# Kernel optimization log

Measured on AMD Instinct MI355X. Metric: run time of the kernel, lower is better.

The kernel has to match this reference:

```python
import jax, jax.numpy as jnp
import numpy as np

# Dimensions (match init_kwargs / input_specs)
B, C, H, W = 16, 16, 64, 64
N = H * W          # num_nodes
D_E = 64           # node_embed_dim
D_H = 128          # gnn_hidden_dim
D_R = 256          # readout_output_dim


def _param(key, shape, fan_in):
    return jax.random.normal(key, shape, jnp.float32) * (1.0 / np.sqrt(fan_in))


def setup_inputs() -> dict:
    key = jax.random.key(0)
    ks = jax.random.split(key, 16)
    inp = {
        "obs": jax.random.normal(ks[0], (B, C, H, W), jnp.float32),
        # node_embedding MLP (2 layers: C -> D_E -> D_E)
        "e1_w": _param(ks[1], (C, D_E), C),   "e1_b": jnp.zeros((D_E,), jnp.float32),
        "e2_w": _param(ks[2], (D_E, D_E), D_E), "e2_b": jnp.zeros((D_E,), jnp.float32),
        # 3 GNN layers (Linear then adjacency aggregation)
        "g1_w": _param(ks[3], (D_E, D_H), D_E), "g1_b": jnp.zeros((D_H,), jnp.float32),
        "g2_w": _param(ks[4], (D_H, D_H), D_H), "g2_b": jnp.zeros((D_H,), jnp.float32),
        "g3_w": _param(ks[5], (D_H, D_H), D_H), "g3_b": jnp.zeros((D_H,), jnp.float32),
        # readout MLP (2 layers: D_H -> 2*D_H -> D_R)
        "r1_w": _param(ks[6], (D_H, 2 * D_H), D_H),   "r1_b": jnp.zeros((2 * D_H,), jnp.float32),
        "r2_w": _param(ks[7], (2 * D_H, D_R), 2 * D_H), "r2_b": jnp.zeros((D_R,), jnp.float32),
    }
    return inp


def _adj_norm():
    # 4-neighbor grid adjacency on an H x W grid, row-normalized (same for every
    # batch element, so build once as (N, N) instead of (B, N, N)).
    idx = jnp.arange(N)
    up = jnp.eye(N, k=-W, dtype=jnp.float32)                      # i > 0
    down = jnp.eye(N, k=W, dtype=jnp.float32)                     # i < H-1
    left = jnp.eye(N, k=-1, dtype=jnp.float32) * ((idx % W) != 0)[:, None]
    right = jnp.eye(N, k=1, dtype=jnp.float32) * ((idx % W) != (W - 1))[:, None]
    adj = up + down + left + right
    return adj / (adj.sum(axis=1, keepdims=True) + 1e-6)


def reference(obs, e1_w, e1_b, e2_w, e2_b,
              g1_w, g1_b, g2_w, g2_b, g3_w, g3_b,
              r1_w, r1_b, r2_w, r2_b):
    relu = jax.nn.relu
    # grid -> graph: (B, C, H, W) -> (B, N, C)
    x = jnp.transpose(obs, (0, 2, 3, 1)).reshape(B, N, C)
    # node embedding MLP (output activation per ding MLP default)
    h = relu(x @ e1_w + e1_b)
    h = relu(h @ e2_w + e2_b)
    A = _adj_norm()  # (N, N)
    for Wg, bg in ((g1_w, g1_b), (g2_w, g2_b), (g3_w, g3_b)):
        support = h @ Wg + bg                      # (B, N, D_H)
        h = relu(jnp.einsum('nm,bmf->bnf', A, support))
    g = h.mean(axis=1)                              # (B, D_H) graph readout
    g = relu(g @ r1_w + r1_b)
    return relu(g @ r2_w + r2_b)                    # (B, D_R)
```

## Files before the change

### kernel.cpp

```cpp
#include <hip/hip_runtime.h>


typedef __attribute__((ext_vector_type(8))) short bf16x8;
typedef __attribute__((ext_vector_type(4))) float f32x4;
#define MFMA(a, b, c) __builtin_amdgcn_mfma_f32_16x16x32_bf16(a, b, c, 0, 0, 0)

__device__ inline void block_sync_lgkm() {
    asm volatile("" ::: "memory");
    __builtin_amdgcn_s_waitcnt(0xC07F);
    __builtin_amdgcn_s_barrier();
    asm volatile("" ::: "memory");
}

__device__ inline ushort bf16h(float x) {
    unsigned u = __float_as_uint(x);
    return (ushort)((u + 0x7fffu + ((u >> 16) & 1u)) >> 16);
}
__device__ inline void split_bf16(float x, ushort& hi, ushort& lo) {
    hi = bf16h(x);
    lo = bf16h(x - __uint_as_float(((unsigned)hi) << 16));
}
__device__ inline unsigned pack_split(float x) {
    unsigned u = __float_as_uint(x);
    unsigned hi = (u + 0x7fffu + ((u >> 16) & 1u)) >> 16;
    float r = x - __uint_as_float(hi << 16);
    return (hi << 16) | (__float_as_uint(r) >> 16);
}
__device__ inline void frag_packed(const unsigned* bp, bf16x8& bh, bf16x8& bl) {
    unsigned p[8];
#pragma unroll
    for (int j = 0; j < 8; j++) p[j] = bp[j * 65];
    union { bf16x8 v; unsigned d[4]; } H, L;
#pragma unroll
    for (int j = 0; j < 4; j++) {
        const unsigned e = p[2 * j], o = p[2 * j + 1];
        H.d[j] = (o & 0xFFFF0000u) | (e >> 16);
        L.d[j] = (o << 16) | (e & 0xFFFFu);
    }
    bh = H.v; bl = L.v;
}

__global__ __launch_bounds__(64) void wprep_kernel(
    const float* __restrict__ e1w, const float* __restrict__ e2w,
    const float* __restrict__ g1w, const float* __restrict__ g2w,
    const float* __restrict__ g3w, ushort* __restrict__ wf,
    float* __restrict__ gsum)
{
    const int blk = blockIdx.x, l = threadIdx.x;
    if (blk >= 92) {
        gsum[(blk - 92) * 64 + l] = 0.f;
        return;
    }
    const float* src; int K, N, kc, t; ushort* dst;
    if (blk < 4)        { src = e1w; K = 16;  N = 64;  kc = 0; t = blk;      dst = wf; }
    else if (blk < 12)  { src = e2w; K = 64;  N = 64;  int u = blk - 4;  kc = u >> 2; t = u & 3; dst = wf + 4096; }
    else if (blk < 28)  { src = g1w; K = 64;  N = 128; int u = blk - 12; kc = u >> 3; t = u & 7; dst = wf + 12288; }
    else if (blk < 60)  { src = g2w; K = 128; N = 128; int u = blk - 28; kc = u >> 3; t = u & 7; dst = wf + 28672; }
    else                { src = g3w; K = 128; N = 128; int u = blk - 60; kc = u >> 3; t = u & 7; dst = wf + 61440; }
    const int T = (N == 64) ? 4 : 8;
    ushort* uh = dst + ((kc * T + t) * 2 + 0) * 512 + l * 8;
    ushort* ul = dst + ((kc * T + t) * 2 + 1) * 512 + l * 8;
    const int f = t * 16 + (l & 15);
    const int kb = kc * 32 + ((l >> 4) << 3);
#pragma unroll
    for (int j = 0; j < 8; j++) {
        const int k = kb + j;
        const float w = (k < K) ? src[k * N + f] : 0.f;
        ushort hi, lo; split_bf16(w, hi, lo);
        uh[j] = hi; ul[j] = lo;
    }
}

__global__ __launch_bounds__(256, 4) void embed_kernel(
    const float* __restrict__ obs, const ushort* __restrict__ wf,
    const float* __restrict__ e1b, const float* __restrict__ e2b,
    float* __restrict__ h0)
{
    __shared__ unsigned Xs[32 * 65];
    __shared__ unsigned Hs[64 * 65];
    const int tid = threadIdx.x, b = blockIdx.x >> 6, row = blockIdx.x & 63;
    const int lane = tid & 63, w = tid >> 6, quad = lane >> 4, nl = lane & 15;
    const int cp = tid >> 4, nq = tid & 15;

    const float4 x4 = *(const float4*)(obs + ((size_t)(b * 16 + cp) << 12) + row * 64 + nq * 4);
    unsigned* xp = Xs + cp * 65 + nq * 4;
    xp[0] = pack_split(x4.x); xp[1] = pack_split(x4.y);
    xp[2] = pack_split(x4.z); xp[3] = pack_split(x4.w);
    unsigned* zp = Xs + (16 + cp) * 65 + nq * 4;
    zp[0] = 0u; zp[1] = 0u; zp[2] = 0u; zp[3] = 0u;
    __syncthreads();

    {
        const ushort* wp = wf + lane * 8;
        const bf16x8 wh = *(const bf16x8*)(wp + (w * 2) * 512);
        const bf16x8 wl = *(const bf16x8*)(wp + (w * 2 + 1) * 512);
#pragma unroll
        for (int nt = 0; nt < 4; nt++) {
            const unsigned* bp = Xs + (quad * 8) * 65 + nt * 16 + nl;
            bf16x8 bh, bl; frag_packed(bp, bh, bl);
            f32x4 c = {0.f, 0.f, 0.f, 0.f};
            c = MFMA(wh, bh, c); c = MFMA(wh, bl, c); c = MFMA(wl, bh, c);
#pragma unroll
            for (int reg = 0; reg < 4; reg++) {
                const int fm = 16 * w + quad * 4 + reg;
                Hs[fm * 65 + nt * 16 + nl] = pack_split(fmaxf(c[reg] + e1b[fm], 0.f));
            }
        }
    }
    __syncthreads();

    const ushort* e2f = wf + 4096;
    f32x4 a2[4];
#pragma unroll
    for (int nt = 0; nt < 4; nt++) a2[nt] = (f32x4){0.f, 0.f, 0.f, 0.f};
#pragma unroll
    for (int kc = 0; kc < 2; kc++) {
        const ushort* wp = e2f + lane * 8;
        const bf16x8 wh = *(const bf16x8*)(wp + ((kc * 4 + w) * 2) * 512);
        const bf16x8 wl = *(const bf16x8*)(wp + ((kc * 4 + w) * 2 + 1) * 512);
#pragma unroll
        for (int nt = 0; nt < 4; nt++) {
            const unsigned* bp = Hs + (kc * 32 + quad * 8) * 65 + nt * 16 + nl;
            bf16x8 bh, bl; frag_packed(bp, bh, bl);
            a2[nt] = MFMA(wh, bh, a2[nt]);
            a2[nt] = MFMA(wh, bl, a2[nt]);
            a2[nt] = MFMA(wl, bh, a2[nt]);
        }
    }
#pragma unroll
    for (int reg = 0; reg < 4; reg++) {
        const int f = 16 * w + quad * 4 + reg;
        const float bv = e2b[f];
#pragma unroll
        for (int nt = 0; nt < 4; nt++)
            h0[((size_t)(b * 64 + f) << 12) + row * 64 + nt * 16 + nl] =
                fmaxf(a2[nt][reg] + bv, 0.f);
    }
}

template <int K, bool MEAN>
__global__ __launch_bounds__(256, 4) void gnn_kernel(
    const float* __restrict__ hin, const ushort* __restrict__ wf,
    const float* __restrict__ bias, float* __restrict__ hout,
    float* __restrict__ gsum)
{
    constexpr int NQ = K / 32;
    __shared__ unsigned As[2][32 * 65];
    const int tid = threadIdx.x;
    const int bid = ((blockIdx.x & 7) << 7) | (blockIdx.x >> 3);
    const int b = bid >> 6, row = bid & 63;
    const int lane = tid & 63, w = tid >> 6, quad = lane >> 4, nl = lane & 15;
    const int kp = tid >> 4, nq = tid & 15;
    const float* hb = hin + (size_t)b * K * 4096;
    const int rowu = (row > 0) ? row - 1 : row;
    const int rowd = (row < 63) ? row + 1 : row;
    const float su = (row > 0) ? 1.f : 0.f;
    const float sd = (row < 63) ? 1.f : 0.f;
    float inv[4];
#pragma unroll
    for (int i = 0; i < 4; i++) {
        const int n = nq * 4 + i;
        const int deg = (row > 0) + (row < 63) + (n > 0) + (n < 63);
        inv[i] = 1.f / ((float)deg + 1e-6f);
    }

    const ushort* wfl = wf + lane * 8;
    f32x4 acc[4][2];
#pragma unroll
    for (int nt = 0; nt < 4; nt++) {
        acc[nt][0] = (f32x4){0.f, 0.f, 0.f, 0.f};
        acc[nt][1] = (f32x4){0.f, 0.f, 0.f, 0.f};
    }

    float4 S[2][6];
    bf16x8 V[2][2];

    auto sload = [&](int s, int q) {
#pragma unroll
        for (int it = 0; it < 2; it++) {
            const int kg = q * 32 + it * 16 + kp;
            const float* pk = hb + ((size_t)kg << 12) + nq * 4;
            S[s][it * 3 + 0] = *(const float4*)(pk + row * 64);
            S[s][it * 3 + 1] = *(const float4*)(pk + rowu * 64);
            S[s][it * 3 + 2] = *(const float4*)(pk + rowd * 64);
        }
    };
    auto wload = [&](int q) {
#pragma unroll
        for (int ftl = 0; ftl < 2; ftl++) {
            V[ftl][0] = *(const bf16x8*)(wfl + ((q * 8 + 2 * w + ftl) * 2) * 512);
            V[ftl][1] = *(const bf16x8*)(wfl + ((q * 8 + 2 * w + ftl) * 2 + 1) * 512);
        }
    };
    auto stage = [&](int s, unsigned* Ab) {
#pragma unroll
        for (int it = 0; it < 2; it++) {
            const int kl = it * 16 + kp;
            const float4 c4 = S[s][it * 3 + 0];
            const float4 u4 = S[s][it * 3 + 1];
            const float4 d4 = S[s][it * 3 + 2];
            const float pw = __shfl_up(c4.w, 1);
            const float nx = __shfl_down(c4.x, 1);
            const float lx = (nq > 0) ? pw : 0.f;
            const float rw = (nq < 15) ? nx : 0.f;
            unsigned* ap = Ab + kl * 65 + nq * 4;
            ap[0] = pack_split((su * u4.x + sd * d4.x + lx + c4.y) * inv[0]);
            ap[1] = pack_split((su * u4.y + sd * d4.y + c4.x + c4.z) * inv[1]);
            ap[2] = pack_split((su * u4.z + sd * d4.z + c4.y + c4.w) * inv[2]);
            ap[3] = pack_split((su * u4.w + sd * d4.w + c4.z + rw) * inv[3]);
        }
    };
    auto consume = [&](const unsigned* Ab) {
#pragma unroll
        for (int nt = 0; nt < 4; nt++) {
            const unsigned* bp = Ab + (quad * 8) * 65 + nt * 16 + nl;
            bf16x8 bh, bl; frag_packed(bp, bh, bl);
            acc[nt][0] = MFMA(V[0][0], bh, acc[nt][0]);
            acc[nt][0] = MFMA(V[0][0], bl, acc[nt][0]);
            acc[nt][0] = MFMA(V[0][1], bh, acc[nt][0]);
            acc[nt][1] = MFMA(V[1][0], bh, acc[nt][1]);
            acc[nt][1] = MFMA(V[1][0], bl, acc[nt][1]);
            acc[nt][1] = MFMA(V[1][1], bh, acc[nt][1]);
        }
    };

    wload(0);
    sload(0, 0);
    sload(1, 1);
    stage(0, As[0]);
    block_sync_lgkm();

#pragma unroll
    for (int q = 0; q < NQ; q++) {
        if (q + 2 < NQ) sload(q & 1, q + 2);
        consume(As[q & 1]);
        if (q + 1 < NQ) {
            wload(q + 1);
            stage((q + 1) & 1, As[(q + 1) & 1]);
            block_sync_lgkm();
        }
    }

    if (!MEAN) {
#pragma unroll
        for (int ftl = 0; ftl < 2; ftl++) {
            const int fb = 32 * w + 16 * ftl + quad * 4;
            const float b0 = bias[fb], b1 = bias[fb + 1], b2 = bias[fb + 2], b3 = bias[fb + 3];
#pragma unroll
            for (int nt = 0; nt < 4; nt++) {
                const int n = 16 * nt + nl;
                const int deg = (row > 0) + (row < 63) + (n > 0) + (n < 63);
                const float rs = (float)deg / ((float)deg + 1e-6f);
                float* op = hout + ((size_t)(b * 128 + fb) << 12) + row * 64 + n;
                op[0]        = fmaxf(acc[nt][ftl][0] + rs * b0, 0.f);
                op[1u << 12] = fmaxf(acc[nt][ftl][1] + rs * b1, 0.f);
                op[2u << 12] = fmaxf(acc[nt][ftl][2] + rs * b2, 0.f);
                op[3u << 12] = fmaxf(acc[nt][ftl][3] + rs * b3, 0.f);
            }
        }
    } else {
#pragma unroll
        for (int ftl = 0; ftl < 2; ftl++) {
            const int fb = 32 * w + 16 * ftl + quad * 4;
#pragma unroll
            for (int reg = 0; reg < 4; reg++) {
                const float bv = bias[fb + reg];
                float v = 0.f;
#pragma unroll
                for (int nt = 0; nt < 4; nt++) {
                    const int n = 16 * nt + nl;
                    const int deg = (row > 0) + (row < 63) + (n > 0) + (n < 63);
                    const float rs = (float)deg / ((float)deg + 1e-6f);
                    v += fmaxf(acc[nt][ftl][reg] + rs * bv, 0.f);
                }
                v += __shfl_xor(v, 1); v += __shfl_xor(v, 2);
                v += __shfl_xor(v, 4); v += __shfl_xor(v, 8);
                if (nl == 0) atomicAdd(&gsum[b * 128 + fb + reg], v * (1.f / 4096.f));
            }
        }
    }
}

__global__ __launch_bounds__(256) void readout_kernel(
    const float* __restrict__ gsum, const float* __restrict__ r1w,
    const float* __restrict__ r1b, const float* __restrict__ r2w,
    const float* __restrict__ r2b, float* __restrict__ out)
{
    __shared__ float gs[128];
    __shared__ float g2[256];
    const int b = blockIdx.x, tid = threadIdx.x;
    if (tid < 128) gs[tid] = gsum[b * 128 + tid];
    __syncthreads();
    float a = r1b[tid];
#pragma unroll 16
    for (int k = 0; k < 128; k++) a = fmaf(gs[k], r1w[k * 256 + tid], a);
    g2[tid] = fmaxf(a, 0.f);
    __syncthreads();
    float a2 = r2b[tid];
#pragma unroll 16
    for (int k = 0; k < 256; k++) a2 = fmaf(g2[k], r2w[k * 256 + tid], a2);
    out[b * 256 + tid] = fmaxf(a2, 0.f);
}

extern "C" void kernel_launch(void* const* d_in, const int* in_sizes, int n_in,
                              void* d_out, int out_size, void* d_ws, size_t ws_size,
                              hipStream_t stream)
{
    const float* obs = (const float*)d_in[0];
    const float* e1w = (const float*)d_in[1];
    const float* e1b = (const float*)d_in[2];
    const float* e2w = (const float*)d_in[3];
    const float* e2b = (const float*)d_in[4];
    const float* g1w = (const float*)d_in[5];
    const float* g1b = (const float*)d_in[6];
    const float* g2w = (const float*)d_in[7];
    const float* g2b = (const float*)d_in[8];
    const float* g3w = (const float*)d_in[9];
    const float* g3b = (const float*)d_in[10];
    const float* r1w = (const float*)d_in[11];
    const float* r1b = (const float*)d_in[12];
    const float* r2w = (const float*)d_in[13];
    const float* r2b = (const float*)d_in[14];
    float* out = (float*)d_out;
    float* ws = (float*)d_ws;

    float* h0 = ws;
    float* h1 = ws + 4194304;
    float* h2 = ws + 4194304 + 8388608;
    float* gsum = (float*)((char*)d_ws + 80u * 1024u * 1024u);
    ushort* wfb = (ushort*)((char*)d_ws + 80u * 1024u * 1024u + 8192u);

    hipLaunchKernelGGL(wprep_kernel, dim3(124), dim3(64), 0, stream,
                       e1w, e2w, g1w, g2w, g3w, wfb, gsum);
    hipLaunchKernelGGL(embed_kernel, dim3(1024), dim3(256), 0, stream,
                       obs, wfb, e1b, e2b, h0);
    hipLaunchKernelGGL((gnn_kernel<64, false>), dim3(1024), dim3(256), 0, stream,
                       h0, wfb + 12288, g1b, h1, nullptr);
    hipLaunchKernelGGL((gnn_kernel<128, false>), dim3(1024), dim3(256), 0, stream,
                       h1, wfb + 28672, g2b, h2, nullptr);
    hipLaunchKernelGGL((gnn_kernel<128, true>), dim3(1024), dim3(256), 0, stream,
                       h2, wfb + 61440, g3b, nullptr, gsum);
    hipLaunchKernelGGL(readout_kernel, dim3(16), dim3(256), 0, stream,
                       gsum, r1w, r1b, r2w, r2b, out);
}
```

Before: 161.5 us.

## Fuse weight prep into embed kernel and single-buffer GNN prefetch registers

Merges the weight-preparation launch and the embedding launch into one kernel. The first blocks convert the GNN weights and zero gsum, and every embedding block loads e1/e2 weights into LDS and splits them into bf16 hi/lo fragments itself. This removes one kernel launch and its dependency gap, at the cost of redundant per-block weight conversion. Separately, the GNN kernel's prefetch buffer shrinks from two register sets to one by reordering the load after staging, which cuts register pressure but shortens the distance between prefetch and use.

After: 160.4 us. About the same (-0.6%).

```diff
diff --git a/kernel.cpp b/kernel.cpp
--- a/kernel.cpp
+++ b/kernel.cpp
@@ -40,91 +40,118 @@
     bh = H.v; bl = L.v;
 }
 
-__global__ __launch_bounds__(64) void wprep_kernel(
-    const float* __restrict__ e1w, const float* __restrict__ e2w,
+__global__ __launch_bounds__(256, 4) void prep_embed_kernel(
+    const float* __restrict__ obs,
+    const float* __restrict__ e1w, const float* __restrict__ e1b,
+    const float* __restrict__ e2w, const float* __restrict__ e2b,
     const float* __restrict__ g1w, const float* __restrict__ g2w,
     const float* __restrict__ g3w, ushort* __restrict__ wf,
-    float* __restrict__ gsum)
+    float* __restrict__ gsum, float* __restrict__ h0)
 {
-    const int blk = blockIdx.x, l = threadIdx.x;
-    if (blk >= 92) {
-        gsum[(blk - 92) * 64 + l] = 0.f;
+    const int blk = blockIdx.x, tid = threadIdx.x;
+
+    if (blk < 20) {
+        const int u = blk * 4 + (tid >> 6);
+        const int l = tid & 63;
+        const float* src; int K, kc, t; ushort* dst;
+        if (u < 16)      { src = g1w; K = 64;  kc = u >> 3;        t = u & 7; dst = wf + 12288; }
+        else if (u < 48) { src = g2w; K = 128; kc = (u - 16) >> 3; t = (u - 16) & 7; dst = wf + 28672; }
+        else             { src = g3w; K = 128; kc = (u - 48) >> 3; t = (u - 48) & 7; dst = wf + 61440; }
+        ushort* uh = dst + ((kc * 8 + t) * 2 + 0) * 512 + l * 8;
+        ushort* ul = dst + ((kc * 8 + t) * 2 + 1) * 512 + l * 8;
+        const int f = t * 16 + (l & 15);
+        const int kb = kc * 32 + ((l >> 4) << 3);
+#pragma unroll
+        for (int j = 0; j < 8; j++) {
+            const int k = kb + j;
+            const float w = (k < K) ? src[k * 128 + f] : 0.f;
+            ushort hi, lo; split_bf16(w, hi, lo);
+            uh[j] = hi; ul[j] = lo;
+        }
         return;
     }
-    const float* src; int K, N, kc, t; ushort* dst;
-    if (blk < 4)        { src = e1w; K = 16;  N = 64;  kc = 0; t = blk;      dst = wf; }
-    else if (blk < 12)  { src = e2w; K = 64;  N = 64;  int u = blk - 4;  kc = u >> 2; t = u & 3; dst = wf + 4096; }
-    else if (blk < 28)  { src = g1w; K = 64;  N = 128; int u = blk - 12; kc = u >> 3; t = u & 7; dst = wf + 12288; }
-    else if (blk < 60)  { src = g2w; K = 128; N = 128; int u = blk - 28; kc = u >> 3; t = u & 7; dst = wf + 28672; }
-    else                { src = g3w; K = 128; N = 128; int u = blk - 60; kc = u >> 3; t = u & 7; dst = wf + 61440; }
-    const int T = (N == 64) ? 4 : 8;
-    ushort* uh = dst + ((kc * T + t) * 2 + 0) * 512 + l * 8;
-    ushort* ul = dst + ((kc * T + t) * 2 + 1) * 512 + l * 8;
-    const int f = t * 16 + (l & 15);
-    const int kb = kc * 32 + ((l >> 4) << 3);
-#pragma unroll
-    for (int j = 0; j < 8; j++) {
-        const int k = kb + j;
-        const float w = (k < K) ? src[k * N + f] : 0.f;
-        ushort hi, lo; split_bf16(w, hi, lo);
-        uh[j] = hi; ul[j] = lo;
-    }
-}
-
-__global__ __launch_bounds__(256, 4) void embed_kernel(
-    const float* __restrict__ obs, const ushort* __restrict__ wf,
-    const float* __restrict__ e1b, const float* __restrict__ e2b,
-    float* __restrict__ h0)
-{
-    __shared__ unsigned Xs[32 * 65];
-    __shared__ unsigned Hs[64 * 65];
-    const int tid = threadIdx.x, b = blockIdx.x >> 6, row = blockIdx.x & 63;
+    if (blk < 28) {
+        gsum[(blk - 20) * 256 + tid] = 0.f;
+        return;
+    }
+
+    __shared__ unsigned lds[6240];
+    const int eb = blk - 28, b = eb >> 6, row = eb & 63;
     const int lane = tid & 63, w = tid >> 6, quad = lane >> 4, nl = lane & 15;
     const int cp = tid >> 4, nq = tid & 15;
 
     const float4 x4 = *(const float4*)(obs + ((size_t)(b * 16 + cp) << 12) + row * 64 + nq * 4);
-    unsigned* xp = Xs + cp * 65 + nq * 4;
-    xp[0] = pack_split(x4.x); xp[1] = pack_split(x4.y);
-    xp[2] = pack_split(x4.z); xp[3] = pack_split(x4.w);
-    unsigned* zp = Xs + (16 + cp) * 65 + nq * 4;
-    zp[0] = 0u; zp[1] = 0u; zp[2] = 0u; zp[3] = 0u;
-    __syncthreads();
 
     {
-        const ushort* wp = wf + lane * 8;
-        const bf16x8 wh = *(const bf16x8*)(wp + (w * 2) * 512);
-        const bf16x8 wl = *(const bf16x8*)(wp + (w * 2 + 1) * 512);
-#pragma unroll
-        for (int nt = 0; nt < 4; nt++) {
-            const unsigned* bp = Xs + (quad * 8) * 65 + nt * 16 + nl;
-            bf16x8 bh, bl; frag_packed(bp, bh, bl);
-            f32x4 c = {0.f, 0.f, 0.f, 0.f};
-            c = MFMA(wh, bh, c); c = MFMA(wh, bl, c); c = MFMA(wl, bh, c);
-#pragma unroll
-            for (int reg = 0; reg < 4; reg++) {
-                const int fm = 16 * w + quad * 4 + reg;
-                Hs[fm * 65 + nt * 16 + nl] = pack_split(fmaxf(c[reg] + e1b[fm], 0.f));
+        float* wr = (float*)lds;
+#pragma unroll
+        for (int i = 0; i < 20; i++) {
+            const int idx = tid + 256 * i;
+            wr[idx] = (idx < 1024) ? e1w[idx] : e2w[idx - 1024];
+        }
+    }
+    __syncthreads();
+
+    bf16x8 e1h, e1l, e2h[2], e2l[2];
+    {
+        const float* wr = (const float*)lds;
+        const int f = 16 * w + nl;
+#pragma unroll
+        for (int j = 0; j < 8; j++) {
+            const int k = quad * 8 + j;
+            const float v = (k < 16) ? wr[k * 64 + f] : 0.f;
+            ushort hi, lo; split_bf16(v, hi, lo);
+            e1h[j] = (short)hi; e1l[j] = (short)lo;
+        }
+#pragma unroll
+        for (int kc = 0; kc < 2; kc++)
+#pragma unroll
+            for (int j = 0; j < 8; j++) {
+                const int k = kc * 32 + quad * 8 + j;
+                const float v = wr[1024 + k * 64 + f];
+                ushort hi, lo; split_bf16(v, hi, lo);
+                e2h[kc][j] = (short)hi; e2l[kc][j] = (short)lo;
             }
-        }
-    }
-    __syncthreads();
-
-    const ushort* e2f = wf + 4096;
+    }
+    __syncthreads();
+
+    unsigned* Xs = lds;
+    unsigned* Hs = lds + 2080;
+    {
+        unsigned* xp = Xs + cp * 65 + nq * 4;
+        xp[0] = pack_split(x4.x); xp[1] = pack_split(x4.y);
+        xp[2] = pack_split(x4.z); xp[3] = pack_split(x4.w);
+        unsigned* zp = Xs + (16 + cp) * 65 + nq * 4;
+        zp[0] = 0u; zp[1] = 0u; zp[2] = 0u; zp[3] = 0u;
+    }
+    __syncthreads();
+
+#pragma unroll
+    for (int nt = 0; nt < 4; nt++) {
+        const unsigned* bp = Xs + (quad * 8) * 65 + nt * 16 + nl;
+        bf16x8 bh, bl; frag_packed(bp, bh, bl);
+        f32x4 c = {0.f, 0.f, 0.f, 0.f};
+        c = MFMA(e1h, bh, c); c = MFMA(e1h, bl, c); c = MFMA(e1l, bh, c);
+#pragma unroll
+        for (int reg = 0; reg < 4; reg++) {
+            const int fm = 16 * w + quad * 4 + reg;
+            Hs[fm * 65 + nt * 16 + nl] = pack_split(fmaxf(c[reg] + e1b[fm], 0.f));
+        }
+    }
+    __syncthreads();
+
     f32x4 a2[4];
 #pragma unroll
     for (int nt = 0; nt < 4; nt++) a2[nt] = (f32x4){0.f, 0.f, 0.f, 0.f};
 #pragma unroll
     for (int kc = 0; kc < 2; kc++) {
-        const ushort* wp = e2f + lane * 8;
-        const bf16x8 wh = *(const bf16x8*)(wp + ((kc * 4 + w) * 2) * 512);
-        const bf16x8 wl = *(const bf16x8*)(wp + ((kc * 4 + w) * 2 + 1) * 512);
 #pragma unroll
         for (int nt = 0; nt < 4; nt++) {
             const unsigned* bp = Hs + (kc * 32 + quad * 8) * 65 + nt * 16 + nl;
             bf16x8 bh, bl; frag_packed(bp, bh, bl);
-            a2[nt] = MFMA(wh, bh, a2[nt]);
-            a2[nt] = MFMA(wh, bl, a2[nt]);
-            a2[nt] = MFMA(wl, bh, a2[nt]);
+            a2[nt] = MFMA(e2h[kc], bh, a2[nt]);
+            a2[nt] = MFMA(e2h[kc], bl, a2[nt]);
+            a2[nt] = MFMA(e2l[kc], bh, a2[nt]);
         }
     }
 #pragma unroll
@@ -172,17 +199,17 @@
         acc[nt][1] = (f32x4){0.f, 0.f, 0.f, 0.f};
     }
 
-    float4 S[2][6];
+    float4 S[6];
     bf16x8 V[2][2];
 
-    auto sload = [&](int s, int q) {
+    auto sload = [&](int q) {
 #pragma unroll
         for (int it = 0; it < 2; it++) {
             const int kg = q * 32 + it * 16 + kp;
             const float* pk = hb + ((size_t)kg << 12) + nq * 4;
-            S[s][it * 3 + 0] = *(const float4*)(pk + row * 64);
-            S[s][it * 3 + 1] = *(const float4*)(pk + rowu * 64);
-            S[s][it * 3 + 2] = *(const float4*)(pk + rowd * 64);
+            S[it * 3 + 0] = *(const float4*)(pk + row * 64);
+            S[it * 3 + 1] = *(const float4*)(pk + rowu * 64);
+            S[it * 3 + 2] = *(const float4*)(pk + rowd * 64);
         }
     };
     auto wload = [&](int q) {
@@ -192,13 +219,13 @@
             V[ftl][1] = *(const bf16x8*)(wfl + ((q * 8 + 2 * w + ftl) * 2 + 1) * 512);
         }
     };
-    auto stage = [&](int s, unsigned* Ab) {
+    auto stage = [&](unsigned* Ab) {
 #pragma unroll
         for (int it = 0; it < 2; it++) {
             const int kl = it * 16 + kp;
-            const float4 c4 = S[s][it * 3 + 0];
-            const float4 u4 = S[s][it * 3 + 1];
-            const float4 d4 = S[s][it * 3 + 2];
+            const float4 c4 = S[it * 3 + 0];
+            const float4 u4 = S[it * 3 + 1];
+            const float4 d4 = S[it * 3 + 2];
             const float pw = __shfl_up(c4.w, 1);
             const float nx = __shfl_down(c4.x, 1);
             const float lx = (nq > 0) ? pw : 0.f;
@@ -225,18 +252,18 @@
     };
 
     wload(0);
-    sload(0, 0);
-    sload(1, 1);
-    stage(0, As[0]);
+    sload(0);
+    stage(As[0]);
+    sload(1);
     block_sync_lgkm();
 
 #pragma unroll
     for (int q = 0; q < NQ; q++) {
-        if (q + 2 < NQ) sload(q & 1, q + 2);
         consume(As[q & 1]);
         if (q + 1 < NQ) {
             wload(q + 1);
-            stage((q + 1) & 1, As[(q + 1) & 1]);
+            stage(As[(q + 1) & 1]);
+            if (q + 2 < NQ) sload(q + 2);
             block_sync_lgkm();
         }
     }
@@ -330,10 +357,8 @@
     float* gsum = (float*)((char*)d_ws + 80u * 1024u * 1024u);
     ushort* wfb = (ushort*)((char*)d_ws + 80u * 1024u * 1024u + 8192u);
 
-    hipLaunchKernelGGL(wprep_kernel, dim3(124), dim3(64), 0, stream,
-                       e1w, e2w, g1w, g2w, g3w, wfb, gsum);
-    hipLaunchKernelGGL(embed_kernel, dim3(1024), dim3(256), 0, stream,
-                       obs, wfb, e1b, e2b, h0);
+    hipLaunchKernelGGL(prep_embed_kernel, dim3(1052), dim3(256), 0, stream,
+                       obs, e1w, e1b, e2w, e2b, g1w, g2w, g3w, wfb, gsum, h0);
     hipLaunchKernelGGL((gnn_kernel<64, false>), dim3(1024), dim3(256), 0, stream,
                        h0, wfb + 12288, g1b, h1, nullptr);
     hipLaunchKernelGGL((gnn_kernel<128, false>), dim3(1024), dim3(256), 0, stream,
```

## Split each grid row into two 32-column tiles to double block count

Applied to the files above, without the earlier changes.

Each block in the embed and GNN kernels now handles half a grid row (32 nodes) rather than a full row, so the grid grows from 1024 to 2048 blocks. Shared tiles shrink to 33-column padding and each block holds half as many accumulators. The GNN staging now loads one k-row per thread plus a halo element across the tile boundary, with a shallower prefetch. Launch bounds are raised to 6 blocks per CU, aiming at more occupancy and better latency hiding. The cost is extra halo and up/down-row loads per node, along with a less aggressive software pipeline.

Result: slower. 201.5 us (+24.8%).

```diff
diff --git a/kernel.cpp b/kernel.cpp
--- a/kernel.cpp
+++ b/kernel.cpp
@@ -26,10 +26,11 @@
     float r = x - __uint_as_float(hi << 16);
     return (hi << 16) | (__float_as_uint(r) >> 16);
 }
+template <int ST>
 __device__ inline void frag_packed(const unsigned* bp, bf16x8& bh, bf16x8& bl) {
     unsigned p[8];
 #pragma unroll
-    for (int j = 0; j < 8; j++) p[j] = bp[j * 65];
+    for (int j = 0; j < 8; j++) p[j] = bp[j * ST];
     union { bf16x8 v; unsigned d[4]; } H, L;
 #pragma unroll
     for (int j = 0; j < 4; j++) {
@@ -71,23 +72,27 @@
     }
 }
 
-__global__ __launch_bounds__(256, 4) void embed_kernel(
+__global__ __launch_bounds__(256, 6) void embed_kernel(
     const float* __restrict__ obs, const ushort* __restrict__ wf,
     const float* __restrict__ e1b, const float* __restrict__ e2b,
     float* __restrict__ h0)
 {
-    __shared__ unsigned Xs[32 * 65];
-    __shared__ unsigned Hs[64 * 65];
-    const int tid = threadIdx.x, b = blockIdx.x >> 6, row = blockIdx.x & 63;
+    __shared__ unsigned Xs[32 * 33];
+    __shared__ unsigned Hs[64 * 33];
+    const int blk = blockIdx.x, tid = threadIdx.x;
+    const int bid = ((blk & 7) << 8) | (blk >> 3);
+    const int b = bid >> 7, row = (bid >> 1) & 63, tile = bid & 1;
+    const int gc = tile << 5;
     const int lane = tid & 63, w = tid >> 6, quad = lane >> 4, nl = lane & 15;
     const int cp = tid >> 4, nq = tid & 15;
 
-    const float4 x4 = *(const float4*)(obs + ((size_t)(b * 16 + cp) << 12) + row * 64 + nq * 4);
-    unsigned* xp = Xs + cp * 65 + nq * 4;
-    xp[0] = pack_split(x4.x); xp[1] = pack_split(x4.y);
-    xp[2] = pack_split(x4.z); xp[3] = pack_split(x4.w);
-    unsigned* zp = Xs + (16 + cp) * 65 + nq * 4;
-    zp[0] = 0u; zp[1] = 0u; zp[2] = 0u; zp[3] = 0u;
+    {
+        const float2 x2 = *(const float2*)(obs + ((size_t)(b * 16 + cp) << 12) + row * 64 + gc + nq * 2);
+        Xs[cp * 33 + nq * 2]            = pack_split(x2.x);
+        Xs[cp * 33 + nq * 2 + 1]        = pack_split(x2.y);
+        Xs[(16 + cp) * 33 + nq * 2]     = 0u;
+        Xs[(16 + cp) * 33 + nq * 2 + 1] = 0u;
+    }
     __syncthreads();
 
     {
@@ -95,33 +100,33 @@
         const bf16x8 wh = *(const bf16x8*)(wp + (w * 2) * 512);
         const bf16x8 wl = *(const bf16x8*)(wp + (w * 2 + 1) * 512);
 #pragma unroll
-        for (int nt = 0; nt < 4; nt++) {
-            const unsigned* bp = Xs + (quad * 8) * 65 + nt * 16 + nl;
-            bf16x8 bh, bl; frag_packed(bp, bh, bl);
+        for (int nt = 0; nt < 2; nt++) {
+            const unsigned* bp = Xs + (quad * 8) * 33 + nt * 16 + nl;
+            bf16x8 bh, bl; frag_packed<33>(bp, bh, bl);
             f32x4 c = {0.f, 0.f, 0.f, 0.f};
             c = MFMA(wh, bh, c); c = MFMA(wh, bl, c); c = MFMA(wl, bh, c);
 #pragma unroll
             for (int reg = 0; reg < 4; reg++) {
                 const int fm = 16 * w + quad * 4 + reg;
-                Hs[fm * 65 + nt * 16 + nl] = pack_split(fmaxf(c[reg] + e1b[fm], 0.f));
+                Hs[fm * 33 + nt * 16 + nl] = pack_split(fmaxf(c[reg] + e1b[fm], 0.f));
             }
         }
     }
     __syncthreads();
 
     const ushort* e2f = wf + 4096;
-    f32x4 a2[4];
-#pragma unroll
-    for (int nt = 0; nt < 4; nt++) a2[nt] = (f32x4){0.f, 0.f, 0.f, 0.f};
+    f32x4 a2[2];
+    a2[0] = (f32x4){0.f, 0.f, 0.f, 0.f};
+    a2[1] = (f32x4){0.f, 0.f, 0.f, 0.f};
 #pragma unroll
     for (int kc = 0; kc < 2; kc++) {
         const ushort* wp = e2f + lane * 8;
         const bf16x8 wh = *(const bf16x8*)(wp + ((kc * 4 + w) * 2) * 512);
         const bf16x8 wl = *(const bf16x8*)(wp + ((kc * 4 + w) * 2 + 1) * 512);
 #pragma unroll
-        for (int nt = 0; nt < 4; nt++) {
-            const unsigned* bp = Hs + (kc * 32 + quad * 8) * 65 + nt * 16 + nl;
-            bf16x8 bh, bl; frag_packed(bp, bh, bl);
+        for (int nt = 0; nt < 2; nt++) {
+            const unsigned* bp = Hs + (kc * 32 + quad * 8) * 33 + nt * 16 + nl;
+            bf16x8 bh, bl; frag_packed<33>(bp, bh, bl);
             a2[nt] = MFMA(wh, bh, a2[nt]);
             a2[nt] = MFMA(wh, bl, a2[nt]);
             a2[nt] = MFMA(wl, bh, a2[nt]);
@@ -132,25 +137,27 @@
         const int f = 16 * w + quad * 4 + reg;
         const float bv = e2b[f];
 #pragma unroll
-        for (int nt = 0; nt < 4; nt++)
-            h0[((size_t)(b * 64 + f) << 12) + row * 64 + nt * 16 + nl] =
+        for (int nt = 0; nt < 2; nt++)
+            h0[((size_t)(b * 64 + f) << 12) + row * 64 + gc + nt * 16 + nl] =
                 fmaxf(a2[nt][reg] + bv, 0.f);
     }
 }
 
 template <int K, bool MEAN>
-__global__ __launch_bounds__(256, 4) void gnn_kernel(
+__global__ __launch_bounds__(256, 6) void gnn_kernel(
     const float* __restrict__ hin, const ushort* __restrict__ wf,
     const float* __restrict__ bias, float* __restrict__ hout,
     float* __restrict__ gsum)
 {
     constexpr int NQ = K / 32;
-    __shared__ unsigned As[2][32 * 65];
-    const int tid = threadIdx.x;
-    const int bid = ((blockIdx.x & 7) << 7) | (blockIdx.x >> 3);
-    const int b = bid >> 6, row = bid & 63;
+    __shared__ unsigned As[2][32 * 33];
+    const int blk = blockIdx.x, tid = threadIdx.x;
+    const int bid = ((blk & 7) << 8) | (blk >> 3);
+    const int b = bid >> 7, row = (bid >> 1) & 63, tile = bid & 1;
+    const int gc = tile << 5;
     const int lane = tid & 63, w = tid >> 6, quad = lane >> 4, nl = lane & 15;
-    const int kp = tid >> 4, nq = tid & 15;
+    const int kq = tid >> 3, nq8 = tid & 7, n0 = nq8 * 4;
+    const int hoff = tile ? -1 : 32;
     const float* hb = hin + (size_t)b * K * 4096;
     const int rowu = (row > 0) ? row - 1 : row;
     const int rowd = (row < 63) ? row + 1 : row;
@@ -159,31 +166,29 @@
     float inv[4];
 #pragma unroll
     for (int i = 0; i < 4; i++) {
-        const int n = nq * 4 + i;
+        const int n = gc + n0 + i;
         const int deg = (row > 0) + (row < 63) + (n > 0) + (n < 63);
         inv[i] = 1.f / ((float)deg + 1e-6f);
     }
 
     const ushort* wfl = wf + lane * 8;
-    f32x4 acc[4][2];
-#pragma unroll
-    for (int nt = 0; nt < 4; nt++) {
+    f32x4 acc[2][2];
+#pragma unroll
+    for (int nt = 0; nt < 2; nt++) {
         acc[nt][0] = (f32x4){0.f, 0.f, 0.f, 0.f};
         acc[nt][1] = (f32x4){0.f, 0.f, 0.f, 0.f};
     }
 
-    float4 S[2][6];
+    float4 S0, S1, S2; float S3;
     bf16x8 V[2][2];
 
-    auto sload = [&](int s, int q) {
-#pragma unroll
-        for (int it = 0; it < 2; it++) {
-            const int kg = q * 32 + it * 16 + kp;
-            const float* pk = hb + ((size_t)kg << 12) + nq * 4;
-            S[s][it * 3 + 0] = *(const float4*)(pk + row * 64);
-            S[s][it * 3 + 1] = *(const float4*)(pk + rowu * 64);
-            S[s][it * 3 + 2] = *(const float4*)(pk + rowd * 64);
-        }
+    auto sload = [&](int q) {
+        const int k = q * 32 + kq;
+        const float* pc = hb + ((size_t)k << 12) + row * 64 + gc;
+        S0 = *(const float4*)(pc + n0);
+        S1 = *(const float4*)(hb + ((size_t)k << 12) + rowu * 64 + gc + n0);
+        S2 = *(const float4*)(hb + ((size_t)k << 12) + rowd * 64 + gc + n0);
+        S3 = pc[hoff];
     };
     auto wload = [&](int q) {
 #pragma unroll
@@ -192,29 +197,24 @@
             V[ftl][1] = *(const bf16x8*)(wfl + ((q * 8 + 2 * w + ftl) * 2 + 1) * 512);
         }
     };
-    auto stage = [&](int s, unsigned* Ab) {
-#pragma unroll
-        for (int it = 0; it < 2; it++) {
-            const int kl = it * 16 + kp;
-            const float4 c4 = S[s][it * 3 + 0];
-            const float4 u4 = S[s][it * 3 + 1];
-            const float4 d4 = S[s][it * 3 + 2];
-            const float pw = __shfl_up(c4.w, 1);
-            const float nx = __shfl_down(c4.x, 1);
-            const float lx = (nq > 0) ? pw : 0.f;
-            const float rw = (nq < 15) ? nx : 0.f;
-            unsigned* ap = Ab + kl * 65 + nq * 4;
-            ap[0] = pack_split((su * u4.x + sd * d4.x + lx + c4.y) * inv[0]);
-            ap[1] = pack_split((su * u4.y + sd * d4.y + c4.x + c4.z) * inv[1]);
-            ap[2] = pack_split((su * u4.z + sd * d4.z + c4.y + c4.w) * inv[2]);
-            ap[3] = pack_split((su * u4.w + sd * d4.w + c4.z + rw) * inv[3]);
-        }
+    auto stage = [&](unsigned* Ab) {
+        const float pw = __shfl_up(S0.w, 1);
+        const float nx = __shfl_down(S0.x, 1);
+        const float eL = tile ? S3 : 0.f;
+        const float eR = tile ? 0.f : S3;
+        const float lx = (nq8 > 0) ? pw : eL;
+        const float rw = (nq8 < 7) ? nx : eR;
+        unsigned* ap = Ab + kq * 33 + n0;
+        ap[0] = pack_split((su * S1.x + sd * S2.x + lx + S0.y) * inv[0]);
+        ap[1] = pack_split((su * S1.y + sd * S2.y + S0.x + S0.z) * inv[1]);
+        ap[2] = pack_split((su * S1.z + sd * S2.z + S0.y + S0.w) * inv[2]);
+        ap[3] = pack_split((su * S1.w + sd * S2.w + S0.z + rw) * inv[3]);
     };
     auto consume = [&](const unsigned* Ab) {
 #pragma unroll
-        for (int nt = 0; nt < 4; nt++) {
-            const unsigned* bp = Ab + (quad * 8) * 65 + nt * 16 + nl;
-            bf16x8 bh, bl; frag_packed(bp, bh, bl);
+        for (int nt = 0; nt < 2; nt++) {
+            const unsigned* bp = Ab + (quad * 8) * 33 + nt * 16 + nl;
+            bf16x8 bh, bl; frag_packed<33>(bp, bh, bl);
             acc[nt][0] = MFMA(V[0][0], bh, acc[nt][0]);
             acc[nt][0] = MFMA(V[0][0], bl, acc[nt][0]);
             acc[nt][0] = MFMA(V[0][1], bh, acc[nt][0]);
@@ -225,18 +225,18 @@
     };
 
     wload(0);
-    sload(0, 0);
-    sload(1, 1);
-    stage(0, As[0]);
+    sload(0);
+    stage(As[0]);
+    sload(1);
     block_sync_lgkm();
 
 #pragma unroll
     for (int q = 0; q < NQ; q++) {
-        if (q + 2 < NQ) sload(q & 1, q + 2);
         consume(As[q & 1]);
         if (q + 1 < NQ) {
             wload(q + 1);
-            stage((q + 1) & 1, As[(q + 1) & 1]);
+            stage(As[(q + 1) & 1]);
+            if (q + 2 < NQ) sload(q + 2);
             block_sync_lgkm();
         }
     }
@@ -247,8 +247,8 @@
             const int fb = 32 * w + 16 * ftl + quad * 4;
             const float b0 = bias[fb], b1 = bias[fb + 1], b2 = bias[fb + 2], b3 = bias[fb + 3];
 #pragma unroll
-            for (int nt = 0; nt < 4; nt++) {
-                const int n = 16 * nt + nl;
+            for (int nt = 0; nt < 2; nt++) {
+                const int n = gc + nt * 16 + nl;
                 const int deg = (row > 0) + (row < 63) + (n > 0) + (n < 63);
                 const float rs = (float)deg / ((float)deg + 1e-6f);
                 float* op = hout + ((size_t)(b * 128 + fb) << 12) + row * 64 + n;
@@ -267,8 +267,8 @@
                 const float bv = bias[fb + reg];
                 float v = 0.f;
 #pragma unroll
-                for (int nt = 0; nt < 4; nt++) {
-                    const int n = 16 * nt + nl;
+                for (int nt = 0; nt < 2; nt++) {
+                    const int n = gc + nt * 16 + nl;
                     const int deg = (row > 0) + (row < 63) + (n > 0) + (n < 63);
                     const float rs = (float)deg / ((float)deg + 1e-6f);
                     v += fmaxf(acc[nt][ftl][reg] + rs * bv, 0.f);
@@ -332,13 +332,13 @@
 
     hipLaunchKernelGGL(wprep_kernel, dim3(124), dim3(64), 0, stream,
                        e1w, e2w, g1w, g2w, g3w, wfb, gsum);
-    hipLaunchKernelGGL(embed_kernel, dim3(1024), dim3(256), 0, stream,
+    hipLaunchKernelGGL(embed_kernel, dim3(2048), dim3(256), 0, stream,
                        obs, wfb, e1b, e2b, h0);
-    hipLaunchKernelGGL((gnn_kernel<64, false>), dim3(1024), dim3(256), 0, stream,
+    hipLaunchKernelGGL((gnn_kernel<64, false>), dim3(2048), dim3(256), 0, stream,
                        h0, wfb + 12288, g1b, h1, nullptr);
-    hipLaunchKernelGGL((gnn_kernel<128, false>), dim3(1024), dim3(256), 0, stream,
+    hipLaunchKernelGGL((gnn_kernel<128, false>), dim3(2048), dim3(256), 0, stream,
                        h1, wfb + 28672, g2b, h2, nullptr);
-    hipLaunchKernelGGL((gnn_kernel<128, true>), dim3(1024), dim3(256), 0, stream,
+    hipLaunchKernelGGL((gnn_kernel<128, true>), dim3(2048), dim3(256), 0, stream,
                        h2, wfb + 61440, g3b, nullptr, gsum);
     hipLaunchKernelGGL(readout_kernel, dim3(16), dim3(256), 0, stream,
                        gsum, r1w, r1b, r2w, r2b, out);
```

## Split GNN output features across two blocks and single-buffer the register staging

Applied to the files above, without the earlier changes.

Each GNN block now computes half of the 128 output features, so the grid doubles from 1024 to 2048 blocks, and each wave holds half the accumulators and weight fragments. The register double-buffering of loaded input rows is replaced by a single buffer, reloaded after staging, and launch bounds rise to 6 blocks per CU. The goal is more occupancy and lower register pressure to hide memory latency. The cost is that each block recomputes the same adjacency-aggregated input tile, so input reads and staging work are doubled.

Result: slower. 229.6 us (+42.2%).

```diff
diff --git a/kernel.cpp b/kernel.cpp
--- a/kernel.cpp
+++ b/kernel.cpp
@@ -139,18 +139,20 @@
 }
 
 template <int K, bool MEAN>
-__global__ __launch_bounds__(256, 4) void gnn_kernel(
+__global__ __launch_bounds__(256, 6) void gnn_kernel(
     const float* __restrict__ hin, const ushort* __restrict__ wf,
     const float* __restrict__ bias, float* __restrict__ hout,
     float* __restrict__ gsum)
 {
     constexpr int NQ = K / 32;
     __shared__ unsigned As[2][32 * 65];
-    const int tid = threadIdx.x;
-    const int bid = ((blockIdx.x & 7) << 7) | (blockIdx.x >> 3);
+    const int blk = blockIdx.x, tid = threadIdx.x;
+    const int fh = (blk >> 3) & 1;
+    const int bid = ((blk & 7) << 7) | (blk >> 4);
     const int b = bid >> 6, row = bid & 63;
     const int lane = tid & 63, w = tid >> 6, quad = lane >> 4, nl = lane & 15;
     const int kp = tid >> 4, nq = tid & 15;
+    const int t = fh * 4 + w;
     const float* hb = hin + (size_t)b * K * 4096;
     const int rowu = (row > 0) ? row - 1 : row;
     const int rowd = (row < 63) ? row + 1 : row;
@@ -165,40 +167,34 @@
     }
 
     const ushort* wfl = wf + lane * 8;
-    f32x4 acc[4][2];
-#pragma unroll
-    for (int nt = 0; nt < 4; nt++) {
-        acc[nt][0] = (f32x4){0.f, 0.f, 0.f, 0.f};
-        acc[nt][1] = (f32x4){0.f, 0.f, 0.f, 0.f};
-    }
-
-    float4 S[2][6];
-    bf16x8 V[2][2];
-
-    auto sload = [&](int s, int q) {
+    f32x4 acc[4];
+#pragma unroll
+    for (int nt = 0; nt < 4; nt++) acc[nt] = (f32x4){0.f, 0.f, 0.f, 0.f};
+
+    float4 S[6];
+    bf16x8 V[2];
+
+    auto sload = [&](int q) {
 #pragma unroll
         for (int it = 0; it < 2; it++) {
             const int kg = q * 32 + it * 16 + kp;
             const float* pk = hb + ((size_t)kg << 12) + nq * 4;
-            S[s][it * 3 + 0] = *(const float4*)(pk + row * 64);
-            S[s][it * 3 + 1] = *(const float4*)(pk + rowu * 64);
-            S[s][it * 3 + 2] = *(const float4*)(pk + rowd * 64);
+            S[it * 3 + 0] = *(const float4*)(pk + row * 64);
+            S[it * 3 + 1] = *(const float4*)(pk + rowu * 64);
+            S[it * 3 + 2] = *(const float4*)(pk + rowd * 64);
         }
     };
     auto wload = [&](int q) {
-#pragma unroll
-        for (int ftl = 0; ftl < 2; ftl++) {
-            V[ftl][0] = *(const bf16x8*)(wfl + ((q * 8 + 2 * w + ftl) * 2) * 512);
-            V[ftl][1] = *(const bf16x8*)(wfl + ((q * 8 + 2 * w + ftl) * 2 + 1) * 512);
-        }
+        V[0] = *(const bf16x8*)(wfl + ((q * 8 + t) * 2) * 512);
+        V[1] = *(const bf16x8*)(wfl + ((q * 8 + t) * 2 + 1) * 512);
     };
-    auto stage = [&](int s, unsigned* Ab) {
+    auto stage = [&](unsigned* Ab) {
 #pragma unroll
         for (int it = 0; it < 2; it++) {
             const int kl = it * 16 + kp;
-            const float4 c4 = S[s][it * 3 + 0];
-            const float4 u4 = S[s][it * 3 + 1];
-            const float4 d4 = S[s][it * 3 + 2];
+            const float4 c4 = S[it * 3 + 0];
+            const float4 u4 = S[it * 3 + 1];
+            const float4 d4 = S[it * 3 + 2];
             const float pw = __shfl_up(c4.w, 1);
             const float nx = __shfl_down(c4.x, 1);
             const float lx = (nq > 0) ? pw : 0.f;
@@ -215,68 +211,58 @@
         for (int nt = 0; nt < 4; nt++) {
             const unsigned* bp = Ab + (quad * 8) * 65 + nt * 16 + nl;
             bf16x8 bh, bl; frag_packed(bp, bh, bl);
-            acc[nt][0] = MFMA(V[0][0], bh, acc[nt][0]);
-            acc[nt][0] = MFMA(V[0][0], bl, acc[nt][0]);
-            acc[nt][0] = MFMA(V[0][1], bh, acc[nt][0]);
-            acc[nt][1] = MFMA(V[1][0], bh, acc[nt][1]);
-            acc[nt][1] = MFMA(V[1][0], bl, acc[nt][1]);
-            acc[nt][1] = MFMA(V[1][1], bh, acc[nt][1]);
+            acc[nt] = MFMA(V[0], bh, acc[nt]);
+            acc[nt] = MFMA(V[0], bl, acc[nt]);
+            acc[nt] = MFMA(V[1], bh, acc[nt]);
         }
     };
 
     wload(0);
-    sload(0, 0);
-    sload(1, 1);
-    stage(0, As[0]);
+    sload(0);
+    stage(As[0]);
+    sload(1);
     block_sync_lgkm();
 
 #pragma unroll
     for (int q = 0; q < NQ; q++) {
-        if (q + 2 < NQ) sload(q & 1, q + 2);
         consume(As[q & 1]);
         if (q + 1 < NQ) {
             wload(q + 1);
-            stage((q + 1) & 1, As[(q + 1) & 1]);
+            stage(As[(q + 1) & 1]);
+            if (q + 2 < NQ) sload(q + 2);
             block_sync_lgkm();
         }
     }
 
+    const int fb = fh * 64 + 16 * w + quad * 4;
     if (!MEAN) {
-#pragma unroll
-        for (int ftl = 0; ftl < 2; ftl++) {
-            const int fb = 32 * w + 16 * ftl + quad * 4;
-            const float b0 = bias[fb], b1 = bias[fb + 1], b2 = bias[fb + 2], b3 = bias[fb + 3];
+        const float b0 = bias[fb], b1 = bias[fb + 1], b2 = bias[fb + 2], b3 = bias[fb + 3];
+#pragma unroll
+        for (int nt = 0; nt < 4; nt++) {
+            const int n = 16 * nt + nl;
+            const int deg = (row > 0) + (row < 63) + (n > 0) + (n < 63);
+            const float rs = (float)deg / ((float)deg + 1e-6f);
+            float* op = hout + ((size_t)(b * 128 + fb) << 12) + row * 64 + n;
+            op[0]        = fmaxf(acc[nt][0] + rs * b0, 0.f);
+            op[1u << 12] = fmaxf(acc[nt][1] + rs * b1, 0.f);
+            op[2u << 12] = fmaxf(acc[nt][2] + rs * b2, 0.f);
+            op[3u << 12] = fmaxf(acc[nt][3] + rs * b3, 0.f);
+        }
+    } else {
+#pragma unroll
+        for (int reg = 0; reg < 4; reg++) {
+            const float bv = bias[fb + reg];
+            float v = 0.f;
 #pragma unroll
             for (int nt = 0; nt < 4; nt++) {
                 const int n = 16 * nt + nl;
                 const int deg = (row > 0) + (row < 63) + (n > 0) + (n < 63);
                 const float rs = (float)deg / ((float)deg + 1e-6f);
-                float* op = hout + ((size_t)(b * 128 + fb) << 12) + row * 64 + n;
-                op[0]        = fmaxf(acc[nt][ftl][0] + rs * b0, 0.f);
-                op[1u << 12] = fmaxf(acc[nt][ftl][1] + rs * b1, 0.f);
-                op[2u << 12] = fmaxf(acc[nt][ftl][2] + rs * b2, 0.f);
-                op[3u << 12] = fmaxf(acc[nt][ftl][3] + rs * b3, 0.f);
+                v += fmaxf(acc[nt][reg] + rs * bv, 0.f);
             }
-        }
-    } else {
-#pragma unroll
-        for (int ftl = 0; ftl < 2; ftl++) {
-            const int fb = 32 * w + 16 * ftl + quad * 4;
-#pragma unroll
-            for (int reg = 0; reg < 4; reg++) {
-                const float bv = bias[fb + reg];
-                float v = 0.f;
-#pragma unroll
-                for (int nt = 0; nt < 4; nt++) {
-                    const int n = 16 * nt + nl;
-                    const int deg = (row > 0) + (row < 63) + (n > 0) + (n < 63);
-                    const float rs = (float)deg / ((float)deg + 1e-6f);
-                    v += fmaxf(acc[nt][ftl][reg] + rs * bv, 0.f);
-                }
-                v += __shfl_xor(v, 1); v += __shfl_xor(v, 2);
-                v += __shfl_xor(v, 4); v += __shfl_xor(v, 8);
-                if (nl == 0) atomicAdd(&gsum[b * 128 + fb + reg], v * (1.f / 4096.f));
-            }
+            v += __shfl_xor(v, 1); v += __shfl_xor(v, 2);
+            v += __shfl_xor(v, 4); v += __shfl_xor(v, 8);
+            if (nl == 0) atomicAdd(&gsum[b * 128 + fb + reg], v * (1.f / 4096.f));
         }
     }
 }
@@ -334,11 +320,11 @@
                        e1w, e2w, g1w, g2w, g3w, wfb, gsum);
     hipLaunchKernelGGL(embed_kernel, dim3(1024), dim3(256), 0, stream,
                        obs, wfb, e1b, e2b, h0);
-    hipLaunchKernelGGL((gnn_kernel<64, false>), dim3(1024), dim3(256), 0, stream,
+    hipLaunchKernelGGL((gnn_kernel<64, false>), dim3(2048), dim3(256), 0, stream,
                        h0, wfb + 12288, g1b, h1, nullptr);
-    hipLaunchKernelGGL((gnn_kernel<128, false>), dim3(1024), dim3(256), 0, stream,
+    hipLaunchKernelGGL((gnn_kernel<128, false>), dim3(2048), dim3(256), 0, stream,
                        h1, wfb + 28672, g2b, h2, nullptr);
-    hipLaunchKernelGGL((gnn_kernel<128, true>), dim3(1024), dim3(256), 0, stream,
+    hipLaunchKernelGGL((gnn_kernel<128, true>), dim3(2048), dim3(256), 0, stream,
                        h2, wfb + 61440, g3b, nullptr, gsum);
     hipLaunchKernelGGL(readout_kernel, dim3(16), dim3(256), 0, stream,
                        gsum, r1w, r1b, r2w, r2b, out);
```
